# Kernel optimization log

Measured on AMD Instinct MI355X. Metric: run time of the kernel, lower is better.

## Reference

```python
import jax, jax.numpy as jnp
import numpy as np

B = 8192      # graphs per batch
NPG = 40      # nodes per graph (= average_nodes, uniform here)
DEG = 16      # avg degree
IN = 64
HID = 32
OUT = 10
K1 = 20       # ceil(0.5*40)
K2 = 10       # ceil(0.5*20)
N = B * NPG
E = N * DEG
EPS = 1e-15


def _lin_params(k, fi, fo):
    kw, kb = jax.random.split(k)
    s = 1.0 / np.sqrt(fi)
    w = jax.random.uniform(kw, (fi, fo), jnp.float32, -s, s)
    b = jax.random.uniform(kb, (fo,), jnp.float32, -s, s)
    return w, b


def setup_inputs():
    key = jax.random.key(0)
    ks = jax.random.split(key, 14)
    x = jax.random.normal(ks[0], (N, IN), jnp.float32)
    # edges constrained within each graph (graphs are contiguous blocks of NPG nodes)
    g = jnp.repeat(jnp.arange(B, dtype=jnp.int32), NPG * DEG)
    src = g * NPG + jax.random.randint(ks[1], (E,), 0, NPG, dtype=jnp.int32)
    dst = g * NPG + jax.random.randint(ks[2], (E,), 0, NPG, dtype=jnp.int32)
    edge_index = jnp.stack([src, dst])
    batch = jnp.repeat(jnp.arange(B, dtype=jnp.int32), NPG)
    w_c1, b_c1 = _lin_params(ks[3], IN, HID)
    w_p1, b_p1 = _lin_params(ks[4], HID, K1)
    w2r, b2 = _lin_params(ks[5], HID, HID)
    w2o, _ = _lin_params(ks[6], HID, HID)
    w_p2, b_p2 = _lin_params(ks[7], HID, K2)
    w3r, b3 = _lin_params(ks[8], HID, HID)
    w3o, _ = _lin_params(ks[9], HID, HID)
    w_l1, b_l1 = _lin_params(ks[10], HID, HID)
    w_l2, b_l2 = _lin_params(ks[11], HID, OUT)
    return dict(x=x, edge_index=edge_index, batch=batch,
                w_c1=w_c1, b_c1=b_c1, w_p1=w_p1, b_p1=b_p1,
                w2r=w2r, b2=b2, w2o=w2o, w_p2=w_p2, b_p2=b_p2,
                w3r=w3r, b3=b3, w3o=w3o,
                w_l1=w_l1, b_l1=b_l1, w_l2=w_l2, b_l2=b_l2)


def _gcn_conv(x, edge_index, w, b):
    # PyG GCNConv: x' = D^-1/2 (A + I) D^-1/2 (X W) + b, unit edge weights
    h = x @ w
    row, col = edge_index
    deg = jnp.zeros((N,), h.dtype).at[col].add(1.0) + 1.0  # +1 self loop
    dinv = jax.lax.rsqrt(deg)
    msg = (dinv[row] * dinv[col])[:, None] * h[row]
    out = jnp.zeros_like(h).at[col].add(msg)
    out = out + (dinv * dinv)[:, None] * h  # self-loop contribution
    return out + b


def _dense_mincut_pool(x, adj, s, mask=None):
    # faithful to torch_geometric.nn.dense_mincut_pool
    s = jax.nn.softmax(s, axis=-1)
    if mask is not None:
        m = mask[..., None].astype(x.dtype)
        x = x * m
        s = s * m
    k = s.shape[-1]
    out = jnp.einsum('bnk,bnf->bkf', s, x)
    out_adj = jnp.einsum('bnk,bnm,bml->bkl', s, adj, s)
    mincut_num = jnp.trace(out_adj, axis1=1, axis2=2)
    d_flat = adj.sum(-1)                                   # [B, n]
    mincut_den = jnp.einsum('bnk,bn,bnk->b', s, d_flat, s)  # tr(S^T D S)
    mincut_loss = jnp.mean(-(mincut_num / mincut_den))
    ss = jnp.einsum('bnk,bnl->bkl', s, s)
    ss_norm = jnp.sqrt(jnp.sum(ss * ss, axis=(1, 2), keepdims=True))
    i_s = jnp.eye(k, dtype=x.dtype) / jnp.sqrt(jnp.asarray(k, x.dtype))
    ortho_loss = jnp.mean(jnp.sqrt(jnp.sum((ss / ss_norm - i_s) ** 2, axis=(1, 2))))
    # zero diagonal, then symmetric degree-normalize coarse adjacency
    eye = jnp.eye(k, dtype=x.dtype)
    out_adj = out_adj * (1.0 - eye)
    d = jnp.sqrt(out_adj.sum(-1))[:, None, :] + EPS        # [B,1,k]
    out_adj = out_adj / d / jnp.swapaxes(d, 1, 2)
    return out, out_adj, mincut_loss, ortho_loss


def _dense_graph_conv(x, adj, w_rel, b, w_root):
    # PyG DenseGraphConv (aggr='add'): lin_rel(A @ x) + lin_root(x); lin_root bias=False
    return (adj @ x) @ w_rel + b + x @ w_root


def reference(x, edge_index, batch, w_c1, b_c1, w_p1, b_p1, w2r, b2, w2o,
              w_p2, b_p2, w3r, b3, w3o, w_l1, b_l1, w_l2, b_l2):
    h = jax.nn.relu(_gcn_conv(x, edge_index, w_c1, b_c1))
    # to_dense_batch (uniform NPG nodes per graph, batch sorted)
    local = jnp.arange(N, dtype=jnp.int32) - batch * NPG
    xd = jnp.zeros((B, NPG, HID), h.dtype).at[batch, local].set(h)
    mask = jnp.ones((B, NPG), bool)
    # to_dense_adj (accumulates duplicate edges)
    row, col = edge_index
    g = batch[row]
    adj = jnp.zeros((B, NPG, NPG), h.dtype).at[g, row - g * NPG, col - g * NPG].add(1.0)
    s = xd @ w_p1 + b_p1
    xd, adj, mc1, o1 = _dense_mincut_pool(xd, adj, s, mask)
    xd = jax.nn.relu(_dense_graph_conv(xd, adj, w2r, b2, w2o))
    s = xd @ w_p2 + b_p2
    xd, adj, mc2, o2 = _dense_mincut_pool(xd, adj, s)
    xd = _dense_graph_conv(xd, adj, w3r, b3, w3o)
    pooled = xd.mean(axis=1)
    out = jax.nn.relu(pooled @ w_l1 + b_l1) @ w_l2 + b_l2
    return out, mc1 + mc2 + o1 + o2
```

## Files before the change

### kernel.cpp

```cpp
#include <hip/hip_runtime.h>

#define NT 256

constexpr int Bg   = 8192;
constexpr int NPG  = 40;
constexpr int EPG  = 640;
constexpr int IN_  = 64;
constexpr int HID  = 32;
constexpr int K1   = 20;
constexpr int K2   = 10;
constexpr int OUTC = 10;
constexpr int NE   = Bg * NPG * 16;
constexpr int SH   = 36;
constexpr float EPSF = 1e-15f;

#define FMA4(acc, a, b) do { \
    float _s = (a); \
    acc.x = fmaf(_s, (b).x, acc.x); \
    acc.y = fmaf(_s, (b).y, acc.y); \
    acc.z = fmaf(_s, (b).z, acc.z); \
    acc.w = fmaf(_s, (b).w, acc.w); } while (0)

__device__ __forceinline__ float wave_red(float v) {
#pragma unroll
    for (int off = 32; off > 0; off >>= 1) v += __shfl_down(v, off, 64);
    return v;
}

__global__ __launch_bounds__(NT, 4)
void mincut_fused(const float* __restrict__ x, const int* __restrict__ ei,
                  const float* __restrict__ w_c1, const float* __restrict__ b_c1,
                  const float* __restrict__ w_p1, const float* __restrict__ b_p1,
                  const float* __restrict__ w2r_, const float* __restrict__ b2_,
                  const float* __restrict__ w2o_,
                  const float* __restrict__ w_p2, const float* __restrict__ b_p2,
                  const float* __restrict__ w3r_, const float* __restrict__ b3_,
                  const float* __restrict__ w3o_,
                  const float* __restrict__ w_l1, const float* __restrict__ b_l1,
                  const float* __restrict__ w_l2, const float* __restrict__ b_l2,
                  float* __restrict__ out, float* __restrict__ wsg)
{
    __shared__ __align__(16) float sA[NPG * NPG];
    __shared__ __align__(16) float sB[2000];
    __shared__ __align__(16) float sXd[NPG * SH];
    __shared__ __align__(16) float sdinv[NPG];
    __shared__ __align__(16) float srowsA[NPG];
    __shared__ __align__(16) float srowm[NPG];
    __shared__ __align__(16) float sden[NPG];
    __shared__ __align__(16) float sc[8];

    float* sA2  = sA;
    float* sX2  = sA + 400;
    float* sA3  = sA + 400;
    float* sH   = sB;
    float* sS   = sB;
    float* sAS  = sB + 800;
    float* sS2  = sB + 800;
    float* sAS2 = sB + 1000;
    float* sX3  = sB + 1200;
    float* sX4  = sB + 1200;
    float* sSS  = sB + 1600;
    float* sXw2r= sXd;
    float* sXw2o= sXd + 720;
    float* sW3r = sXd;
    float* sW3o = sXd + 360;

    const int g    = blockIdx.x;
    const int tid  = threadIdx.x;
    const int lane = tid & 63;
    const int wid  = tid >> 6;

    int er0, ec0, er1, ec1, er2 = -1, ec2 = 0;
    {
        const int eb = g * EPG, nb = g * NPG;
        int e = eb + tid;
        er0 = ei[e] - nb; ec0 = ei[NE + e] - nb;
        e += NT;
        er1 = ei[e] - nb; ec1 = ei[NE + e] - nb;
        if (tid + 2 * NT < EPG) {
            e += NT;
            er2 = ei[e] - nb; ec2 = ei[NE + e] - nb;
        }
    }
    for (int i = tid; i < NPG * NPG; i += NT) sA[i] = 0.f;
    __syncthreads();

    atomicAdd(&sA[er0 * NPG + ec0], 1.f);
    atomicAdd(&sA[er1 * NPG + ec1], 1.f);
    if (er2 >= 0) atomicAdd(&sA[er2 * NPG + ec2], 1.f);

    float4 hacc0 = {0.f,0.f,0.f,0.f}, hacc1 = {0.f,0.f,0.f,0.f};
    if (tid < 160) {
        int np = tid >> 3, fq = tid & 7;
        int n0 = 2 * np, n1 = n0 + 1;
        const float4* x0 = (const float4*)(x + (size_t)g * (NPG * IN_) + n0 * IN_);
        const float4* x1 = (const float4*)(x + (size_t)g * (NPG * IN_) + n1 * IN_);
        const float4* wg = (const float4*)w_c1;
#pragma unroll 4
        for (int kk = 0; kk < IN_ / 4; kk++) {
            float4 a0 = x0[kk], a1 = x1[kk];
            float4 w0 = wg[(4*kk+0)*8 + fq];
            float4 w1 = wg[(4*kk+1)*8 + fq];
            float4 w2 = wg[(4*kk+2)*8 + fq];
            float4 w3 = wg[(4*kk+3)*8 + fq];
            FMA4(hacc0, a0.x, w0); FMA4(hacc0, a0.y, w1);
            FMA4(hacc0, a0.z, w2); FMA4(hacc0, a0.w, w3);
            FMA4(hacc1, a1.x, w0); FMA4(hacc1, a1.y, w1);
            FMA4(hacc1, a1.z, w2); FMA4(hacc1, a1.w, w3);
        }
    }
    __syncthreads();

    if (tid < 160) {
        int np = tid >> 3, fq = tid & 7;
        int n0 = 2 * np, n1 = n0 + 1;
        ((float4*)(sH + n0 * SH))[fq] = hacc0;
        ((float4*)(sH + n1 * SH))[fq] = hacc1;
    } else if (tid >= 192 && tid < 202) {
        int c0 = 4 * (tid - 192);
        float4 s = {0.f,0.f,0.f,0.f};
#pragma unroll 8
        for (int r = 0; r < NPG; r++) {
            float4 a = *(const float4*)&sA[r * NPG + c0];
            s.x += a.x; s.y += a.y; s.z += a.z; s.w += a.w;
        }
        sdinv[c0+0] = rsqrtf(s.x + 1.f);
        sdinv[c0+1] = rsqrtf(s.y + 1.f);
        sdinv[c0+2] = rsqrtf(s.z + 1.f);
        sdinv[c0+3] = rsqrtf(s.w + 1.f);
    } else if (tid >= 202 && tid < 212) {
        int r0 = 4 * (tid - 202);
        float s0 = 0.f, s1 = 0.f, s2 = 0.f, s3 = 0.f;
#pragma unroll
        for (int j = 0; j < 10; j++) {
            float4 a0 = *(const float4*)&sA[(r0+0) * NPG + 4*j];
            float4 a1 = *(const float4*)&sA[(r0+1) * NPG + 4*j];
            float4 a2 = *(const float4*)&sA[(r0+2) * NPG + 4*j];
            float4 a3 = *(const float4*)&sA[(r0+3) * NPG + 4*j];
            s0 += a0.x + a0.y + a0.z + a0.w;
            s1 += a1.x + a1.y + a1.z + a1.w;
            s2 += a2.x + a2.y + a2.z + a2.w;
            s3 += a3.x + a3.y + a3.z + a3.w;
        }
        srowsA[r0+0] = s0; srowsA[r0+1] = s1;
        srowsA[r0+2] = s2; srowsA[r0+3] = s3;
    }
    __syncthreads();

    if (tid < 80) {
        int cp = tid >> 3, fq = tid & 7;
        int c0 = 4 * cp;
        float4 acc0 = {0.f,0.f,0.f,0.f}, acc1 = {0.f,0.f,0.f,0.f};
        float4 acc2 = {0.f,0.f,0.f,0.f}, acc3 = {0.f,0.f,0.f,0.f};
#pragma unroll 8
        for (int r = 0; r < NPG; r++) {
            float4 a = *(const float4*)&sA[r * NPG + c0];
            float dv = sdinv[r];
            float4 bv = ((const float4*)(sH + r * SH))[fq];
            FMA4(acc0, a.x * dv, bv);
            FMA4(acc1, a.y * dv, bv);
            FMA4(acc2, a.z * dv, bv);
            FMA4(acc3, a.w * dv, bv);
        }
        float4 bb = ((const float4*)b_c1)[fq];
#pragma unroll
        for (int i = 0; i < 4; i++) {
            float4 acc = (i == 0) ? acc0 : (i == 1) ? acc1 : (i == 2) ? acc2 : acc3;
            int c = c0 + i;
            float d = sdinv[c];
            float4 h = ((const float4*)(sH + c * SH))[fq];
            float4 r;
            r.x = fmaxf(fmaf(d, fmaf(d, h.x, acc.x), bb.x), 0.f);
            r.y = fmaxf(fmaf(d, fmaf(d, h.y, acc.y), bb.y), 0.f);
            r.z = fmaxf(fmaf(d, fmaf(d, h.z, acc.z), bb.z), 0.f);
            r.w = fmaxf(fmaf(d, fmaf(d, h.w, acc.w), bb.w), 0.f);
            ((float4*)(sXd + c * SH))[fq] = r;
        }
    }
    __syncthreads();

    if (tid < 100) {
        int np = tid / 5, lq = tid - np * 5;
        int n0 = 2 * np, n1 = n0 + 1;
        const float4* wg = (const float4*)w_p1;
        float4 bb = ((const float4*)b_p1)[lq];
        float4 acc0 = bb, acc1 = bb;
#pragma unroll
        for (int j = 0; j < 8; j++) {
            float4 a0 = ((const float4*)(sXd + n0 * SH))[j];
            float4 a1 = ((const float4*)(sXd + n1 * SH))[j];
            float4 w0 = wg[(4*j+0) * 5 + lq];
            float4 w1 = wg[(4*j+1) * 5 + lq];
            float4 w2 = wg[(4*j+2) * 5 + lq];
            float4 w3 = wg[(4*j+3) * 5 + lq];
            FMA4(acc0, a0.x, w0); FMA4(acc0, a0.y, w1);
            FMA4(acc0, a0.z, w2); FMA4(acc0, a0.w, w3);
            FMA4(acc1, a1.x, w0); FMA4(acc1, a1.y, w1);
            FMA4(acc1, a1.z, w2); FMA4(acc1, a1.w, w3);
        }
        ((float4*)(sS + n0 * K1))[lq] = acc0;
        ((float4*)(sS + n1 * K1))[lq] = acc1;
    }
    __syncthreads();

    if (tid < NPG) {
        float4* row4 = (float4*)(sS + tid * K1);
        float4 v[5];
        float m = -3.0e38f;
#pragma unroll
        for (int j = 0; j < 5; j++) {
            v[j] = row4[j];
            m = fmaxf(m, fmaxf(fmaxf(v[j].x, v[j].y), fmaxf(v[j].z, v[j].w)));
        }
        float ssum = 0.f;
#pragma unroll
        for (int j = 0; j < 5; j++) {
            v[j].x = __expf(v[j].x - m); v[j].y = __expf(v[j].y - m);
            v[j].z = __expf(v[j].z - m); v[j].w = __expf(v[j].w - m);
            ssum += v[j].x + v[j].y + v[j].z + v[j].w;
        }
        float inv = 1.f / ssum;
#pragma unroll
        for (int j = 0; j < 5; j++) {
            v[j].x *= inv; v[j].y *= inv; v[j].z *= inv; v[j].w *= inv;
            row4[j] = v[j];
        }
    }
    __syncthreads();

    if (tid < 100) {
        int np = tid / 5, lq = tid - np * 5;
        int n0 = 2 * np, n1 = n0 + 1;
        const float4* sb4 = (const float4*)sS;
        float4 acc0 = {0.f,0.f,0.f,0.f}, acc1 = {0.f,0.f,0.f,0.f};
#pragma unroll
        for (int m4 = 0; m4 < NPG / 4; m4++) {
            float4 a0 = *(const float4*)&sA[n0 * NPG + 4 * m4];
            float4 a1 = *(const float4*)&sA[n1 * NPG + 4 * m4];
            float4 b0 = sb4[(4*m4+0)*5 + lq];
            float4 b1 = sb4[(4*m4+1)*5 + lq];
            float4 b2v = sb4[(4*m4+2)*5 + lq];
            float4 b3v = sb4[(4*m4+3)*5 + lq];
            FMA4(acc0, a0.x, b0); FMA4(acc0, a0.y, b1);
            FMA4(acc0, a0.z, b2v); FMA4(acc0, a0.w, b3v);
            FMA4(acc1, a1.x, b0); FMA4(acc1, a1.y, b1);
            FMA4(acc1, a1.z, b2v); FMA4(acc1, a1.w, b3v);
        }
        ((float4*)(sAS + n0 * K1))[lq] = acc0;
        ((float4*)(sAS + n1 * K1))[lq] = acc1;
    } else if (tid >= 128 && tid < 178) {
        int oo = tid - 128;
        int kp = oo / 5, lq = oo - kp * 5;
        int k0 = 2 * kp, k1 = k0 + 1;
        float4 acc0 = {0.f,0.f,0.f,0.f}, acc1 = {0.f,0.f,0.f,0.f};
#pragma unroll 8
        for (int n = 0; n < NPG; n++) {
            float2 s2v = *(const float2*)&sS[n * K1 + k0];
            float4 bv = ((const float4*)(sS + n * K1))[lq];
            FMA4(acc0, s2v.x, bv); FMA4(acc1, s2v.y, bv);
        }
        ((float4*)(sSS + k0 * K1))[lq] = acc0;
        ((float4*)(sSS + k1 * K1))[lq] = acc1;
    }
    __syncthreads();

    if (tid < 25) {
        int kp = tid / 5, lq = tid - kp * 5;
        int k0 = 4 * kp;
        float4 acc0 = {0.f,0.f,0.f,0.f}, acc1 = {0.f,0.f,0.f,0.f};
        float4 acc2 = {0.f,0.f,0.f,0.f}, acc3 = {0.f,0.f,0.f,0.f};
#pragma unroll 8
        for (int n = 0; n < NPG; n++) {
            float4 sv = *(const float4*)&sS[n * K1 + k0];
            float4 bv = ((const float4*)(sAS + n * K1))[lq];
            FMA4(acc0, sv.x, bv); FMA4(acc1, sv.y, bv);
            FMA4(acc2, sv.z, bv); FMA4(acc3, sv.w, bv);
        }
        ((float4*)(sA2 + (k0+0) * K1))[lq] = acc0;
        ((float4*)(sA2 + (k0+1) * K1))[lq] = acc1;
        ((float4*)(sA2 + (k0+2) * K1))[lq] = acc2;
        ((float4*)(sA2 + (k0+3) * K1))[lq] = acc3;
    } else if (tid >= 64 && tid < 104) {
        int oo = tid - 64;
        int kp = oo >> 3, fq = oo & 7;
        int k0 = 4 * kp;
        float4 acc0 = {0.f,0.f,0.f,0.f}, acc1 = {0.f,0.f,0.f,0.f};
        float4 acc2 = {0.f,0.f,0.f,0.f}, acc3 = {0.f,0.f,0.f,0.f};
#pragma unroll 8
        for (int n = 0; n < NPG; n++) {
            float4 sv = *(const float4*)&sS[n * K1 + k0];
            float4 bv = ((const float4*)(sXd + n * SH))[fq];
            FMA4(acc0, sv.x, bv); FMA4(acc1, sv.y, bv);
            FMA4(acc2, sv.z, bv); FMA4(acc3, sv.w, bv);
        }
        ((float4*)(sX2 + (k0+0) * SH))[fq] = acc0;
        ((float4*)(sX2 + (k0+1) * SH))[fq] = acc1;
        ((float4*)(sX2 + (k0+2) * SH))[fq] = acc2;
        ((float4*)(sX2 + (k0+3) * SH))[fq] = acc3;
    } else if (tid >= 128 && tid < 168) {
        int n = tid - 128;
        float s2 = 0.f;
#pragma unroll
        for (int j = 0; j < 5; j++) {
            float4 v = ((const float4*)(sS + n * K1))[j];
            s2 = fmaf(v.x, v.x, s2); s2 = fmaf(v.y, v.y, s2);
            s2 = fmaf(v.z, v.z, s2); s2 = fmaf(v.w, v.w, s2);
        }
        sden[n] = srowsA[n] * s2;
    }
    __syncthreads();

    if (wid == 0) {
        float f = 0.f, tr = 0.f;
        for (int i = lane; i < K1 * K1; i += 64) {
            float t = sSS[i];
            f = fmaf(t, t, f);
            if (i % (K1 + 1) == 0) tr += t;
        }
        f = wave_red(f); tr = wave_red(tr);
        if (lane == 0)
            sc[2] = sqrtf(fmaxf(2.f - 2.f * tr / (sqrtf(f) * 4.47213595499958f), 0.f));
    } else if (wid == 1) {
        float v = 0.f;
        if (lane < K1) {
            float s = 0.f;
#pragma unroll
            for (int j = 0; j < 5; j++) {
                float4 a = *(const float4*)&sA2[lane * K1 + 4*j];
                s += a.x + a.y + a.z + a.w;
            }
            float d = sA2[lane * (K1 + 1)];
            srowm[lane] = 1.f / (sqrtf(s - d) + EPSF);
            v = d;
        }
        v = wave_red(v);
        if (lane == 0) sc[0] = v;
    } else if (wid == 2) {
        float v = (lane < NPG) ? sden[lane] : 0.f;
        v = wave_red(v);
        if (lane == 0) sc[1] = v;
    }
    for (int o = tid; o < 320; o += NT) {
        int first = o < 160; int m = first ? o : o - 160;
        int n = m >> 3, fq = m & 7;
        const float4* wg = (const float4*)(first ? w2r_ : w2o_);
        float4 acc = {0.f,0.f,0.f,0.f};
#pragma unroll
        for (int j = 0; j < 8; j++) {
            float4 a = ((const float4*)(sX2 + n * SH))[j];
            float4 w0 = wg[(4*j+0) * 8 + fq];
            float4 w1 = wg[(4*j+1) * 8 + fq];
            float4 w2 = wg[(4*j+2) * 8 + fq];
            float4 w3 = wg[(4*j+3) * 8 + fq];
            FMA4(acc, a.x, w0); FMA4(acc, a.y, w1);
            FMA4(acc, a.z, w2); FMA4(acc, a.w, w3);
        }
        ((float4*)((first ? sXw2r : sXw2o) + n * SH))[fq] = acc;
    }
    __syncthreads();

    if (tid < 160) {
        int k = tid >> 3, fq = tid & 7;
        float4 a[5];
#pragma unroll
        for (int j = 0; j < 5; j++) {
            float4 av = *(const float4*)&sA2[k * K1 + 4*j];
            float4 rm = *(const float4*)&srowm[4*j];
            a[j].x = av.x * rm.x; a[j].y = av.y * rm.y;
            a[j].z = av.z * rm.z; a[j].w = av.w * rm.w;
        }
        float4 acc = {0.f,0.f,0.f,0.f};
#pragma unroll
        for (int j = 0; j < 5; j++) {
            float4 w0 = ((const float4*)(sXw2r + (4*j+0) * SH))[fq];
            float4 w1 = ((const float4*)(sXw2r + (4*j+1) * SH))[fq];
            float4 w2 = ((const float4*)(sXw2r + (4*j+2) * SH))[fq];
            float4 w3 = ((const float4*)(sXw2r + (4*j+3) * SH))[fq];
            FMA4(acc, a[j].x, w0); FMA4(acc, a[j].y, w1);
            FMA4(acc, a[j].z, w2); FMA4(acc, a[j].w, w3);
        }
        float adiag = sA2[k * (K1 + 1)] * srowm[k];
        float4 wk = ((const float4*)(sXw2r + k * SH))[fq];
        acc.x -= adiag * wk.x; acc.y -= adiag * wk.y;
        acc.z -= adiag * wk.z; acc.w -= adiag * wk.w;
        float4 bb = ((const float4*)b2_)[fq];
        float4 oo = ((const float4*)(sXw2o + k * SH))[fq];
        float rk = srowm[k];
        float4 r;
        r.x = fmaxf(fmaf(rk, acc.x, oo.x + bb.x), 0.f);
        r.y = fmaxf(fmaf(rk, acc.y, oo.y + bb.y), 0.f);
        r.z = fmaxf(fmaf(rk, acc.z, oo.z + bb.z), 0.f);
        r.w = fmaxf(fmaf(rk, acc.w, oo.w + bb.w), 0.f);
        ((float4*)(sX2 + k * SH))[fq] = r;
    }
    __syncthreads();

    if (tid < K1) {
        float acc[K2];
#pragma unroll
        for (int q = 0; q < K2; q++) acc[q] = b_p2[q];
#pragma unroll
        for (int j = 0; j < 8; j++) {
            float4 a = ((const float4*)(sX2 + tid * SH))[j];
#pragma unroll
            for (int q = 0; q < K2; q++) acc[q] = fmaf(a.x, w_p2[(4*j+0) * K2 + q], acc[q]);
#pragma unroll
            for (int q = 0; q < K2; q++) acc[q] = fmaf(a.y, w_p2[(4*j+1) * K2 + q], acc[q]);
#pragma unroll
            for (int q = 0; q < K2; q++) acc[q] = fmaf(a.z, w_p2[(4*j+2) * K2 + q], acc[q]);
#pragma unroll
            for (int q = 0; q < K2; q++) acc[q] = fmaf(a.w, w_p2[(4*j+3) * K2 + q], acc[q]);
        }
        float m = -3.0e38f;
#pragma unroll
        for (int q = 0; q < K2; q++) m = fmaxf(m, acc[q]);
        float ssum = 0.f;
#pragma unroll
        for (int q = 0; q < K2; q++) { acc[q] = __expf(acc[q] - m); ssum += acc[q]; }
        float inv = 1.f / ssum;
#pragma unroll
        for (int q2 = 0; q2 < 5; q2++) {
            float2 wv; wv.x = acc[2*q2] * inv; wv.y = acc[2*q2+1] * inv;
            *(float2*)&sS2[tid * K2 + 2*q2] = wv;
        }
    }
    __syncthreads();

    if (tid < 100) {
        int n = tid / 5, lp = tid - (tid / 5) * 5;
        int l0 = 2 * lp;
        float accx = 0.f, accy = 0.f;
#pragma unroll
        for (int j = 0; j < 5; j++) {
            float4 av = *(const float4*)&sA2[n * K1 + 4*j];
            float4 rm = *(const float4*)&srowm[4*j];
            float2 s0 = *(const float2*)&sS2[(4*j+0) * K2 + l0];
            float2 s1 = *(const float2*)&sS2[(4*j+1) * K2 + l0];
            float2 s2v = *(const float2*)&sS2[(4*j+2) * K2 + l0];
            float2 s3 = *(const float2*)&sS2[(4*j+3) * K2 + l0];
            float c0 = av.x * rm.x, c1 = av.y * rm.y, c2 = av.z * rm.z, c3 = av.w * rm.w;
            accx = fmaf(c0, s0.x, accx); accy = fmaf(c0, s0.y, accy);
            accx = fmaf(c1, s1.x, accx); accy = fmaf(c1, s1.y, accy);
            accx = fmaf(c2, s2v.x, accx); accy = fmaf(c2, s2v.y, accy);
            accx = fmaf(c3, s3.x, accx); accy = fmaf(c3, s3.y, accy);
        }
        float cd = sA2[n * (K1 + 1)] * srowm[n];
        float2 sn = *(const float2*)&sS2[n * K2 + l0];
        accx -= cd * sn.x; accy -= cd * sn.y;
        float rn = srowm[n];
        float2 wv; wv.x = accx * rn; wv.y = accy * rn;
        *(float2*)&sAS2[n * K2 + l0] = wv;
    } else if (tid >= 128 && tid < 153) {
        int oo = tid - 128;
        int kp = oo / 5, lp = oo - kp * 5;
        int k0 = 2 * kp, l0 = 2 * lp;
        float a00 = 0.f, a01 = 0.f, a10 = 0.f, a11 = 0.f;
#pragma unroll
        for (int n = 0; n < K1; n++) {
            float2 a = *(const float2*)&sS2[n * K2 + k0];
            float2 b = *(const float2*)&sS2[n * K2 + l0];
            a00 = fmaf(a.x, b.x, a00); a01 = fmaf(a.x, b.y, a01);
            a10 = fmaf(a.y, b.x, a10); a11 = fmaf(a.y, b.y, a11);
        }
        sSS[(k0+0) * K2 + l0]     = a00;
        sSS[(k0+0) * K2 + l0 + 1] = a01;
        sSS[(k0+1) * K2 + l0]     = a10;
        sSS[(k0+1) * K2 + l0 + 1] = a11;
    } else if (tid >= 160 && tid < 180) {
        int n = tid - 160;
        float da = 0.f;
#pragma unroll
        for (int j = 0; j < 5; j++) {
            float4 av = *(const float4*)&sA2[n * K1 + 4*j];
            float4 rm = *(const float4*)&srowm[4*j];
            da = fmaf(av.x, rm.x, da); da = fmaf(av.y, rm.y, da);
            da = fmaf(av.z, rm.z, da); da = fmaf(av.w, rm.w, da);
        }
        da -= sA2[n * (K1 + 1)] * srowm[n];
        da *= srowm[n];
        float s2 = 0.f;
#pragma unroll
        for (int q2 = 0; q2 < 5; q2++) {
            float2 v = *(const float2*)&sS2[n * K2 + 2*q2];
            s2 = fmaf(v.x, v.x, s2); s2 = fmaf(v.y, v.y, s2);
        }
        sden[n] = da * s2;
    } else if (tid >= 192 && tid < 232) {
        int oo = tid - 192;
        int kp = oo >> 3, fq = oo & 7;
        int k0 = 2 * kp;
        float4 acc0 = {0.f,0.f,0.f,0.f}, acc1 = {0.f,0.f,0.f,0.f};
#pragma unroll
        for (int n = 0; n < K1; n++) {
            float2 sv = *(const float2*)&sS2[n * K2 + k0];
            float4 bv = ((const float4*)(sX2 + n * SH))[fq];
            FMA4(acc0, sv.x, bv); FMA4(acc1, sv.y, bv);
        }
        ((float4*)(sX3 + (k0+0) * SH))[fq] = acc0;
        ((float4*)(sX3 + (k0+1) * SH))[fq] = acc1;
    }
    __syncthreads();

    if (tid < 25) {
        int kp = tid / 5, lp = tid - kp * 5;
        int k0 = 2 * kp, l0 = 2 * lp;
        float a00 = 0.f, a01 = 0.f, a10 = 0.f, a11 = 0.f;
#pragma unroll
        for (int n = 0; n < K1; n++) {
            float2 sv = *(const float2*)&sS2[n * K2 + k0];
            float2 av = *(const float2*)&sAS2[n * K2 + l0];
            a00 = fmaf(sv.x, av.x, a00); a01 = fmaf(sv.x, av.y, a01);
            a10 = fmaf(sv.y, av.x, a10); a11 = fmaf(sv.y, av.y, a11);
        }
        sA3[(k0+0) * K2 + l0]     = a00;
        sA3[(k0+0) * K2 + l0 + 1] = a01;
        sA3[(k0+1) * K2 + l0]     = a10;
        sA3[(k0+1) * K2 + l0 + 1] = a11;
    } else if (wid == 2) {
        float v = (lane < K1) ? sden[lane] : 0.f;
        v = wave_red(v);
        if (lane == 0) sc[5] = v;
    } else if (wid == 3) {
        float f = 0.f, tr = 0.f;
        for (int i = lane; i < K2 * K2; i += 64) {
            float t = sSS[i];
            f = fmaf(t, t, f);
            if (i % (K2 + 1) == 0) tr += t;
        }
        f = wave_red(f); tr = wave_red(tr);
        if (lane == 0)
            sc[6] = sqrtf(fmaxf(2.f - 2.f * tr / (sqrtf(f) * 3.1622776601683795f), 0.f));
    }
    __syncthreads();

    if (tid < 160) {
        bool first = (tid < 80);
        int oo = first ? tid : tid - 80;
        int n = oo >> 3, fq = oo & 7;
        const float4* wg = (const float4*)(first ? w3r_ : w3o_);
        float4 acc = {0.f,0.f,0.f,0.f};
#pragma unroll
        for (int j = 0; j < 8; j++) {
            float4 a = ((const float4*)(sX3 + n * SH))[j];
            float4 w0 = wg[(4*j+0) * 8 + fq];
            float4 w1 = wg[(4*j+1) * 8 + fq];
            float4 w2 = wg[(4*j+2) * 8 + fq];
            float4 w3 = wg[(4*j+3) * 8 + fq];
            FMA4(acc, a.x, w0); FMA4(acc, a.y, w1);
            FMA4(acc, a.z, w2); FMA4(acc, a.w, w3);
        }
        if (first) ((float4*)(sW3r + n * SH))[fq] = acc;
        else       ((float4*)(sW3o + n * SH))[fq] = acc;
    } else if (tid >= 192 && tid < 202) {
        int l = tid - 192;
        float s = 0.f;
#pragma unroll
        for (int j = 0; j < 5; j++) {
            float2 a = *(const float2*)&sA3[l * K2 + 2*j];
            s += a.x + a.y;
        }
        s -= sA3[l * (K2 + 1)];
        srowm[l] = 1.f / (sqrtf(s) + EPSF);
    } else if (tid == 202) {
        float num2 = 0.f;
#pragma unroll
        for (int k = 0; k < K2; k++) num2 += sA3[k * (K2 + 1)];
        wsg[g] = -(sc[0] / sc[1]) + sc[2] - num2 / sc[5] + sc[6];
    }
    __syncthreads();

    if (tid < 80) {
        int k = tid >> 3, fq = tid & 7;
        float4 acc = {0.f,0.f,0.f,0.f};
#pragma unroll
        for (int j = 0; j < 5; j++) {
            float2 av = *(const float2*)&sA3[k * K2 + 2*j];
            float2 rm = *(const float2*)&srowm[2*j];
            float c0 = av.x * rm.x, c1 = av.y * rm.y;
            float4 w0 = ((const float4*)(sW3r + (2*j+0) * SH))[fq];
            float4 w1 = ((const float4*)(sW3r + (2*j+1) * SH))[fq];
            FMA4(acc, c0, w0); FMA4(acc, c1, w1);
        }
        float adiag = sA3[k * (K2 + 1)] * srowm[k];
        float4 wk = ((const float4*)(sW3r + k * SH))[fq];
        acc.x -= adiag * wk.x; acc.y -= adiag * wk.y;
        acc.z -= adiag * wk.z; acc.w -= adiag * wk.w;
        float4 bb = ((const float4*)b3_)[fq];
        float4 oo = ((const float4*)(sW3o + k * SH))[fq];
        float rk = srowm[k];
        float4 r;
        r.x = fmaf(rk, acc.x, oo.x + bb.x);
        r.y = fmaf(rk, acc.y, oo.y + bb.y);
        r.z = fmaf(rk, acc.z, oo.z + bb.z);
        r.w = fmaf(rk, acc.w, oo.w + bb.w);
        ((float4*)(sX4 + k * SH))[fq] = r;
    }
    __syncthreads();

    if (wid == 0) {
        int f = lane & 31;
        float pool = 0.f;
#pragma unroll
        for (int n = 0; n < K2; n++) pool += sX4[n * SH + f];
        pool *= (1.f / K2);
        float acc = b_l1[f];
#pragma unroll
        for (int j = 0; j < HID; j++)
            acc = fmaf(__shfl(pool, j, 64), w_l1[j * HID + f], acc);
        float t1 = fmaxf(acc, 0.f);
        int o = (lane < OUTC) ? lane : 0;
        float acc2 = b_l2[o];
#pragma unroll
        for (int j = 0; j < HID; j++)
            acc2 = fmaf(__shfl(t1, j, 64), w_l2[j * OUTC + o], acc2);
        if (lane < OUTC) out[(size_t)g * OUTC + lane] = acc2;
    }
}

__global__ void loss_reduce(const float* __restrict__ wsg, float* __restrict__ out)
{
    __shared__ float sred[4];
    int tid = threadIdx.x;
    float s = 0.f;
    for (int i = tid; i < Bg; i += NT) s += wsg[i];
    s = wave_red(s);
    if ((tid & 63) == 0) sred[tid >> 6] = s;
    __syncthreads();
    if (tid == 0) out[(size_t)Bg * OUTC] = (sred[0] + sred[1] + sred[2] + sred[3]) * (1.f / Bg);
}

extern "C" void kernel_launch(void* const* d_in, const int* in_sizes, int n_in,
                              void* d_out, int out_size, void* d_ws, size_t ws_size,
                              hipStream_t stream)
{
    const float* x    = (const float*)d_in[0];
    const int*   ei   = (const int*)  d_in[1];
    const float* w_c1 = (const float*)d_in[3];
    const float* b_c1 = (const float*)d_in[4];
    const float* w_p1 = (const float*)d_in[5];
    const float* b_p1 = (const float*)d_in[6];
    const float* w2r  = (const float*)d_in[7];
    const float* b2   = (const float*)d_in[8];
    const float* w2o  = (const float*)d_in[9];
    const float* w_p2 = (const float*)d_in[10];
    const float* b_p2 = (const float*)d_in[11];
    const float* w3r  = (const float*)d_in[12];
    const float* b3   = (const float*)d_in[13];
    const float* w3o  = (const float*)d_in[14];
    const float* w_l1 = (const float*)d_in[15];
    const float* b_l1 = (const float*)d_in[16];
    const float* w_l2 = (const float*)d_in[17];
    const float* b_l2 = (const float*)d_in[18];
    float* out = (float*)d_out;
    float* wsg = (float*)d_ws;

    hipLaunchKernelGGL(mincut_fused, dim3(Bg), dim3(NT), 0, stream,
                       x, ei, w_c1, b_c1, w_p1, b_p1, w2r, b2, w2o,
                       w_p2, b_p2, w3r, b3, w3o, w_l1, b_l1, w_l2, b_l2,
                       out, wsg);
    hipLaunchKernelGGL(loss_reduce, dim3(1), dim3(NT), 0, stream, wsg, out);
}
```

Before: 233.1 us.

## Fuse degree counting into edge atomics and merge pool projection with softmax

Row sums and column degrees are now accumulated with shared-memory atomics during adjacency construction, so the separate reduction pass over the 40x40 adjacency goes away. The H store happens right after the GEMM, and the rsqrt for each degree is computed where it is used. The pool projection and the softmax are merged into one pass where each of 40 threads computes a full 20-wide row in registers, removing two barriers. The cost is three times as many atomics, fewer active threads in the projection (40 instead of 100), higher register use, and repeated rsqrt work.

```diff
diff --git a/kernel.cpp b/kernel.cpp
--- a/kernel.cpp
+++ b/kernel.cpp
@@ -83,19 +83,28 @@
         }
     }
     for (int i = tid; i < NPG * NPG; i += NT) sA[i] = 0.f;
+    if (tid < NPG) { sdinv[tid] = 0.f; srowsA[tid] = 0.f; }
     __syncthreads();
 
     atomicAdd(&sA[er0 * NPG + ec0], 1.f);
+    atomicAdd(&srowsA[er0], 1.f);
+    atomicAdd(&sdinv[ec0], 1.f);
     atomicAdd(&sA[er1 * NPG + ec1], 1.f);
-    if (er2 >= 0) atomicAdd(&sA[er2 * NPG + ec2], 1.f);
-
-    float4 hacc0 = {0.f,0.f,0.f,0.f}, hacc1 = {0.f,0.f,0.f,0.f};
+    atomicAdd(&srowsA[er1], 1.f);
+    atomicAdd(&sdinv[ec1], 1.f);
+    if (er2 >= 0) {
+        atomicAdd(&sA[er2 * NPG + ec2], 1.f);
+        atomicAdd(&srowsA[er2], 1.f);
+        atomicAdd(&sdinv[ec2], 1.f);
+    }
+
     if (tid < 160) {
         int np = tid >> 3, fq = tid & 7;
         int n0 = 2 * np, n1 = n0 + 1;
         const float4* x0 = (const float4*)(x + (size_t)g * (NPG * IN_) + n0 * IN_);
         const float4* x1 = (const float4*)(x + (size_t)g * (NPG * IN_) + n1 * IN_);
         const float4* wg = (const float4*)w_c1;
+        float4 hacc0 = {0.f,0.f,0.f,0.f}, hacc1 = {0.f,0.f,0.f,0.f};
 #pragma unroll 4
         for (int kk = 0; kk < IN_ / 4; kk++) {
             float4 a0 = x0[kk], a1 = x1[kk];
@@ -108,42 +117,8 @@
             FMA4(hacc1, a1.x, w0); FMA4(hacc1, a1.y, w1);
             FMA4(hacc1, a1.z, w2); FMA4(hacc1, a1.w, w3);
         }
-    }
-    __syncthreads();
-
-    if (tid < 160) {
-        int np = tid >> 3, fq = tid & 7;
-        int n0 = 2 * np, n1 = n0 + 1;
         ((float4*)(sH + n0 * SH))[fq] = hacc0;
         ((float4*)(sH + n1 * SH))[fq] = hacc1;
-    } else if (tid >= 192 && tid < 202) {
-        int c0 = 4 * (tid - 192);
-        float4 s = {0.f,0.f,0.f,0.f};
-#pragma unroll 8
-        for (int r = 0; r < NPG; r++) {
-            float4 a = *(const float4*)&sA[r * NPG + c0];
-            s.x += a.x; s.y += a.y; s.z += a.z; s.w += a.w;
-        }
-        sdinv[c0+0] = rsqrtf(s.x + 1.f);
-        sdinv[c0+1] = rsqrtf(s.y + 1.f);
-        sdinv[c0+2] = rsqrtf(s.z + 1.f);
-        sdinv[c0+3] = rsqrtf(s.w + 1.f);
-    } else if (tid >= 202 && tid < 212) {
-        int r0 = 4 * (tid - 202);
-        float s0 = 0.f, s1 = 0.f, s2 = 0.f, s3 = 0.f;
-#pragma unroll
-        for (int j = 0; j < 10; j++) {
-            float4 a0 = *(const float4*)&sA[(r0+0) * NPG + 4*j];
-            float4 a1 = *(const float4*)&sA[(r0+1) * NPG + 4*j];
-            float4 a2 = *(const float4*)&sA[(r0+2) * NPG + 4*j];
-            float4 a3 = *(const float4*)&sA[(r0+3) * NPG + 4*j];
-            s0 += a0.x + a0.y + a0.z + a0.w;
-            s1 += a1.x + a1.y + a1.z + a1.w;
-            s2 += a2.x + a2.y + a2.z + a2.w;
-            s3 += a3.x + a3.y + a3.z + a3.w;
-        }
-        srowsA[r0+0] = s0; srowsA[r0+1] = s1;
-        srowsA[r0+2] = s2; srowsA[r0+3] = s3;
     }
     __syncthreads();
 
@@ -155,7 +130,7 @@
 #pragma unroll 8
         for (int r = 0; r < NPG; r++) {
             float4 a = *(const float4*)&sA[r * NPG + c0];
-            float dv = sdinv[r];
+            float dv = rsqrtf(sdinv[r] + 1.f);
             float4 bv = ((const float4*)(sH + r * SH))[fq];
             FMA4(acc0, a.x * dv, bv);
             FMA4(acc1, a.y * dv, bv);
@@ -167,7 +142,7 @@
         for (int i = 0; i < 4; i++) {
             float4 acc = (i == 0) ? acc0 : (i == 1) ? acc1 : (i == 2) ? acc2 : acc3;
             int c = c0 + i;
-            float d = sdinv[c];
+            float d = rsqrtf(sdinv[c] + 1.f);
             float4 h = ((const float4*)(sH + c * SH))[fq];
             float4 r;
             r.x = fmaxf(fmaf(d, fmaf(d, h.x, acc.x), bb.x), 0.f);
@@ -179,51 +154,36 @@
     }
     __syncthreads();
 
-    if (tid < 100) {
-        int np = tid / 5, lq = tid - np * 5;
-        int n0 = 2 * np, n1 = n0 + 1;
-        const float4* wg = (const float4*)w_p1;
-        float4 bb = ((const float4*)b_p1)[lq];
-        float4 acc0 = bb, acc1 = bb;
+    if (tid < NPG) {
+        float acc[K1];
+#pragma unroll
+        for (int q = 0; q < K1; q++) acc[q] = b_p1[q];
 #pragma unroll
         for (int j = 0; j < 8; j++) {
-            float4 a0 = ((const float4*)(sXd + n0 * SH))[j];
-            float4 a1 = ((const float4*)(sXd + n1 * SH))[j];
-            float4 w0 = wg[(4*j+0) * 5 + lq];
-            float4 w1 = wg[(4*j+1) * 5 + lq];
-            float4 w2 = wg[(4*j+2) * 5 + lq];
-            float4 w3 = wg[(4*j+3) * 5 + lq];
-            FMA4(acc0, a0.x, w0); FMA4(acc0, a0.y, w1);
-            FMA4(acc0, a0.z, w2); FMA4(acc0, a0.w, w3);
-            FMA4(acc1, a1.x, w0); FMA4(acc1, a1.y, w1);
-            FMA4(acc1, a1.z, w2); FMA4(acc1, a1.w, w3);
-        }
-        ((float4*)(sS + n0 * K1))[lq] = acc0;
-        ((float4*)(sS + n1 * K1))[lq] = acc1;
-    }
-    __syncthreads();
-
-    if (tid < NPG) {
+            float4 a = ((const float4*)(sXd + tid * SH))[j];
+#pragma unroll
+            for (int q = 0; q < K1; q++) acc[q] = fmaf(a.x, w_p1[(4*j+0) * K1 + q], acc[q]);
+#pragma unroll
+            for (int q = 0; q < K1; q++) acc[q] = fmaf(a.y, w_p1[(4*j+1) * K1 + q], acc[q]);
+#pragma unroll
+            for (int q = 0; q < K1; q++) acc[q] = fmaf(a.z, w_p1[(4*j+2) * K1 + q], acc[q]);
+#pragma unroll
+            for (int q = 0; q < K1; q++) acc[q] = fmaf(a.w, w_p1[(4*j+3) * K1 + q], acc[q]);
+        }
+        float m = -3.0e38f;
+#pragma unroll
+        for (int q = 0; q < K1; q++) m = fmaxf(m, acc[q]);
+        float ssum = 0.f;
+#pragma unroll
+        for (int q = 0; q < K1; q++) { acc[q] = __expf(acc[q] - m); ssum += acc[q]; }
+        float inv = 1.f / ssum;
         float4* row4 = (float4*)(sS + tid * K1);
-        float4 v[5];
-        float m = -3.0e38f;
-#pragma unroll
-        for (int j = 0; j < 5; j++) {
-            v[j] = row4[j];
-            m = fmaxf(m, fmaxf(fmaxf(v[j].x, v[j].y), fmaxf(v[j].z, v[j].w)));
-        }
-        float ssum = 0.f;
-#pragma unroll
-        for (int j = 0; j < 5; j++) {
-            v[j].x = __expf(v[j].x - m); v[j].y = __expf(v[j].y - m);
-            v[j].z = __expf(v[j].z - m); v[j].w = __expf(v[j].w - m);
-            ssum += v[j].x + v[j].y + v[j].z + v[j].w;
-        }
-        float inv = 1.f / ssum;
-#pragma unroll
-        for (int j = 0; j < 5; j++) {
-            v[j].x *= inv; v[j].y *= inv; v[j].z *= inv; v[j].w *= inv;
-            row4[j] = v[j];
+#pragma unroll
+        for (int q4 = 0; q4 < 5; q4++) {
+            float4 wv;
+            wv.x = acc[4*q4+0] * inv; wv.y = acc[4*q4+1] * inv;
+            wv.z = acc[4*q4+2] * inv; wv.w = acc[4*q4+3] * inv;
+            row4[q4] = wv;
         }
     }
     __syncthreads();
```

Result: slower. 262.7 us (+12.7%).
